# Kernel optimization log

Hardware: AMD Instinct MI355X
Metric: run time of the kernel (lower is better)

## Reference

```python
import jax, jax.numpy as jnp
import numpy as np

NUM_USERS = 100000
NUM_ITEMS = 50000
N_NODES = NUM_USERS + NUM_ITEMS
EMBED_DIM = 64
NUM_LAYERS = 3
NUM_EDGES = 1250000
EDGE_ATTR_DIM = 7
MLP_HID = 32
AUDIO_SCALE = 1.0
META_SCALE = 0.5


def _l2norm(x, eps=1e-12):
    # F.normalize(p=2, dim=-1): x / max(||x||, eps)
    n = jnp.sqrt(jnp.sum(x * x, axis=-1, keepdims=True))
    return x / jnp.maximum(n, eps)


def setup_inputs() -> dict:
    key = jax.random.key(0)
    ks = jax.random.split(key, 12)
    return {
        'user_emb_w': jax.random.normal(ks[0], (NUM_USERS, EMBED_DIM), jnp.float32),
        'artist_emb_w': jax.random.normal(ks[1], (20000, EMBED_DIM), jnp.float32),
        'album_emb_w': jax.random.normal(ks[2], (40000, EMBED_DIM), jnp.float32),
        'item_audio': jax.random.normal(ks[3], (NUM_ITEMS, EMBED_DIM), jnp.float32),
        'edge_attr': jax.random.normal(ks[4], (NUM_EDGES, EDGE_ATTR_DIM), jnp.float32),
        'edge_weight_init': jax.random.uniform(ks[5], (NUM_EDGES,), jnp.float32),
        'w1': jax.random.normal(ks[6], (EDGE_ATTR_DIM + 1, MLP_HID), jnp.float32),
        'b1': jnp.zeros((MLP_HID,), jnp.float32),
        'w2': jax.random.normal(ks[7], (MLP_HID, 1), jnp.float32),
        'b2': jnp.zeros((1,), jnp.float32),
        'edge_index': jax.random.randint(ks[8], (2, NUM_EDGES), 0, N_NODES, jnp.int64 if jax.config.read('jax_enable_x64') else jnp.int32),
        'artist_ids': jax.random.randint(ks[9], (NUM_ITEMS,), 0, 20000, jnp.int32),
        'album_ids': jax.random.randint(ks[10], (NUM_ITEMS,), 0, 40000, jnp.int32),
    }


def reference(user_emb_w, artist_emb_w, album_emb_w, item_audio, edge_attr,
              edge_weight_init, w1, b1, w2, b2, edge_index, artist_ids, album_ids):
    # Edge weight MLP: Linear -> ReLU -> Linear -> Sigmoid, squeezed
    ef = jnp.concatenate([edge_attr, edge_weight_init[:, None]], axis=1)  # [E, 8]
    h = jax.nn.relu(ef @ w1 + b1)
    w = jax.nn.sigmoid(h @ w2 + b2)[:, 0]  # [E]

    # Node features
    user_embed = _l2norm(user_emb_w)                                   # [U, D]
    meta = (artist_emb_w[artist_ids] + album_emb_w[album_ids]) * META_SCALE
    item_embed = _l2norm(item_audio * AUDIO_SCALE + meta)              # [I, D]
    x = jnp.concatenate([user_embed, item_embed], axis=0)              # [N, D]

    # gcn_norm (LGConv default, no self-loops): deg from target (col) scatter of w
    row, col = edge_index[0], edge_index[1]
    deg = jax.ops.segment_sum(w, col, num_segments=N_NODES)
    dinv = jnp.where(deg > 0, jax.lax.rsqrt(jnp.maximum(deg, 1e-30)), 0.0)
    norm = dinv[row] * w * dinv[col]                                   # [E]

    acc = x
    for _ in range(NUM_LAYERS):
        msg = norm[:, None] * x[row]                                   # [E, D]
        x = jax.ops.segment_sum(msg, col, num_segments=N_NODES)       # [N, D]
        acc = acc + x
    x = _l2norm(acc / (NUM_LAYERS + 1))

    user_emb = x[:NUM_USERS]
    item_emb = x[NUM_USERS:]
    align_loss = jnp.float32(0.0)
    return user_emb, item_emb, align_loss
```

## Files before the change

kernel.cpp:

```cpp
#include <hip/hip_runtime.h>
#include <hip/hip_bf16.h>
#include <math.h>

#define NUM_USERS  100000
#define NUM_ITEMS  50000
#define N_NODES    150000
#define EMBED_DIM  64
#define NUM_EDGES  1250000
#define MLP_HID    32
#define SCAN_B     1024
#define SCAN_NB    ((N_NODES + SCAN_B - 1) / SCAN_B)
#define NPW        4
#define PAD(x)     (((x) + 7) & ~7)

__global__ void hist_mlp(const float* __restrict__ edge_attr,
                         const float* __restrict__ ew,
                         const float* __restrict__ w1,
                         const float* __restrict__ b1,
                         const float* __restrict__ w2,
                         const float* __restrict__ b2,
                         const int*   __restrict__ edge_index,
                         int*  __restrict__ cnt,
                         int*  __restrict__ rank,
                         int2* __restrict__ epair) {
    __shared__ float w1s[8 * MLP_HID];
    __shared__ float b1s[MLP_HID];
    __shared__ float w2s[MLP_HID];
    int tid = threadIdx.x;
    if (tid < 8 * MLP_HID) w1s[tid] = w1[tid];
    if (tid < MLP_HID) { b1s[tid] = b1[tid]; w2s[tid] = w2[tid]; }
    __syncthreads();

    int e = blockIdx.x * blockDim.x + tid;
    if (e >= NUM_EDGES) return;

    int c = edge_index[NUM_EDGES + e];
    rank[e] = atomicAdd(&cnt[c], 1);

    float ef[8];
#pragma unroll
    for (int k = 0; k < 7; ++k) ef[k] = edge_attr[e * 7 + k];
    ef[7] = ew[e];

    float s = b2[0];
#pragma unroll
    for (int j = 0; j < MLP_HID; ++j) {
        float h = b1s[j];
#pragma unroll
        for (int k = 0; k < 8; ++k) h = fmaf(ef[k], w1s[k * MLP_HID + j], h);
        h = fmaxf(h, 0.0f);
        s = fmaf(h, w2s[j], s);
    }
    float w = 1.0f / (1.0f + expf(-s));

    int2 pr;
    pr.x = edge_index[e];
    pr.y = __float_as_int(w);
    epair[e] = pr;
}

__global__ void scan_partial(const int* __restrict__ cnt,
                             int* __restrict__ part) {
    __shared__ int s[SCAN_B];
    int tid = threadIdx.x;
    int i = blockIdx.x * SCAN_B + tid;
    s[tid] = (i < N_NODES) ? PAD(cnt[i]) : 0;
    __syncthreads();
#pragma unroll
    for (int off = SCAN_B / 2; off > 0; off >>= 1) {
        if (tid < off) s[tid] += s[tid + off];
        __syncthreads();
    }
    if (tid == 0) part[blockIdx.x] = s[0];
}

__global__ void scan_offsets(const int* __restrict__ part,
                             int* __restrict__ base_off) {
    __shared__ int s[256];
    int tid = threadIdx.x;
    int v = (tid < SCAN_NB) ? part[tid] : 0;
    s[tid] = v;
    __syncthreads();
#pragma unroll
    for (int off = 1; off < 256; off <<= 1) {
        int t = (tid >= off) ? s[tid - off] : 0;
        __syncthreads();
        s[tid] += t;
        __syncthreads();
    }
    if (tid < SCAN_NB) base_off[tid] = s[tid] - v;
}

__global__ void scan_apply(const int* __restrict__ cnt,
                           const int* __restrict__ base_off,
                           int* __restrict__ row_ptr) {
    __shared__ int s[SCAN_B];
    int tid = threadIdx.x;
    int i = blockIdx.x * SCAN_B + tid;
    int v = (i < N_NODES) ? PAD(cnt[i]) : 0;
    s[tid] = v;
    __syncthreads();
    for (int off = 1; off < SCAN_B; off <<= 1) {
        int t = (tid >= off) ? s[tid - off] : 0;
        __syncthreads();
        s[tid] += t;
        __syncthreads();
    }
    if (i < N_NODES) row_ptr[i] = s[tid] - v + base_off[blockIdx.x];
    if (i == N_NODES - 1) row_ptr[N_NODES] = s[tid] + base_off[blockIdx.x];
}

__global__ void scatter_perm(const int* __restrict__ edge_index,
                             const int* __restrict__ rank,
                             const int* __restrict__ row_ptr,
                             int* __restrict__ perm) {
    int e = blockIdx.x * blockDim.x + threadIdx.x;
    if (e >= NUM_EDGES) return;
    int c = edge_index[NUM_EDGES + e];
    perm[row_ptr[c] + rank[e]] = e;
}

__global__ void pair_build(const int* __restrict__ row_ptr,
                           const int* __restrict__ cnt,
                           const int* __restrict__ perm,
                           const int2* __restrict__ epair,
                           int2* __restrict__ csr_pair,
                           float* __restrict__ dinv) {
    int t = blockIdx.x * blockDim.x + threadIdx.x;
    int node = t >> 4;
    int lane = t & 15;
    if (node >= N_NODES) return;
    int s = row_ptr[node];
    int e = row_ptr[node + 1];
    int re = s + cnt[node];
    float sum = 0.0f;
    for (int j = s + lane; j < e; j += 16) {
        int2 pr;
        if (j < re) {
            int eid = perm[j];
            pr = epair[eid];
            sum += __int_as_float(pr.y);
        } else {
            pr.x = 0; pr.y = 0;
        }
        csr_pair[j] = pr;
    }
    sum += __shfl_xor(sum, 8);
    sum += __shfl_xor(sum, 4);
    sum += __shfl_xor(sum, 2);
    sum += __shfl_xor(sum, 1);
    if (lane == 0)
        dinv[node] = (sum > 0.0f) ? rsqrtf(fmaxf(sum, 1e-30f)) : 0.0f;
}

__global__ void init_x(const float* __restrict__ user_w,
                       const float* __restrict__ artist_w,
                       const float* __restrict__ album_w,
                       const float* __restrict__ audio,
                       const int*   __restrict__ artist_ids,
                       const int*   __restrict__ album_ids,
                       __hip_bfloat16* __restrict__ x) {
    int t = blockIdx.x * blockDim.x + threadIdx.x;
    int row = t >> 6;
    int lane = t & 63;
    if (row >= N_NODES) return;

    float v;
    if (row < NUM_USERS) {
        v = user_w[row * EMBED_DIM + lane];
    } else {
        int r = row - NUM_USERS;
        int ar = artist_ids[r];
        int al = album_ids[r];
        v = audio[r * EMBED_DIM + lane]
          + 0.5f * (artist_w[ar * EMBED_DIM + lane] + album_w[al * EMBED_DIM + lane]);
    }
    float ss = v * v;
#pragma unroll
    for (int off = 32; off > 0; off >>= 1) ss += __shfl_xor(ss, off);
    float scale = 1.0f / fmaxf(sqrtf(ss), 1e-12f);
    x[row * EMBED_DIM + lane] = __float2bfloat16(v * scale);
}

#define BF_LO(u) __uint_as_float((u) << 16)
#define BF_HI(u) __uint_as_float((u) & 0xffff0000u)

__global__ void propagate_mid(const int* __restrict__ row_ptr,
                              const int2* __restrict__ csr_pair,
                              const float* __restrict__ dinv,
                              const unsigned short* __restrict__ xin,
                              unsigned short* __restrict__ xout) {
    int wave = (blockIdx.x * blockDim.x + threadIdx.x) >> 6;
    int lane = threadIdx.x & 63;
    int node0 = wave * NPW;
    if (node0 >= N_NODES) return;

    int eg = lane >> 4;
    int dq = (lane & 15) << 2;

    int rpv = row_ptr[node0 + (lane <= NPW ? lane : NPW)];
    int rs0 = __shfl(rpv, 0);
    int rs1 = __shfl(rpv, 1);
    int rs2 = __shfl(rpv, 2);
    int rs3 = __shfl(rpv, 3);
    int rs4 = __shfl(rpv, 4);

    int j = rs0 + eg;
    int2 pa = csr_pair[j];
    int2 pb = csr_pair[j + 4];

#pragma unroll
    for (int k = 0; k < NPW; ++k) {
        int bs = (k == 0) ? rs0 : (k == 1) ? rs1 : (k == 2) ? rs2 : rs3;
        int be = (k == 0) ? rs1 : (k == 1) ? rs2 : (k == 2) ? rs3 : rs4;
        float a0 = 0, a1 = 0, a2 = 0, a3 = 0;

        for (int base = bs; base < be; base += 8) {
            int   sa = pa.x; float wa = __int_as_float(pa.y);
            int   sb = pb.x; float wb = __int_as_float(pb.y);
            float da = dinv[sa];
            float db = dinv[sb];
            uint2 ua = *(const uint2*)(xin + ((size_t)sa << 6) + dq);
            uint2 ub = *(const uint2*)(xin + ((size_t)sb << 6) + dq);

            j += 8;
            pa = csr_pair[j];
            pb = csr_pair[j + 4];

            float fa = wa * da;
            float fb = wb * db;
            a0 = fmaf(fa, BF_LO(ua.x), a0); a1 = fmaf(fa, BF_HI(ua.x), a1);
            a2 = fmaf(fa, BF_LO(ua.y), a2); a3 = fmaf(fa, BF_HI(ua.y), a3);
            a0 = fmaf(fb, BF_LO(ub.x), a0); a1 = fmaf(fb, BF_HI(ub.x), a1);
            a2 = fmaf(fb, BF_LO(ub.y), a2); a3 = fmaf(fb, BF_HI(ub.y), a3);
        }

        a0 += __shfl_xor(a0, 16); a1 += __shfl_xor(a1, 16);
        a2 += __shfl_xor(a2, 16); a3 += __shfl_xor(a3, 16);
        a0 += __shfl_xor(a0, 32); a1 += __shfl_xor(a1, 32);
        a2 += __shfl_xor(a2, 32); a3 += __shfl_xor(a3, 32);

        if (eg == 0) {
            float dc = dinv[node0 + k];
            size_t o = ((size_t)(node0 + k) << 6) + dq;
            unsigned int b0 = (unsigned int)__bfloat16_as_ushort(__float2bfloat16(a0 * dc));
            unsigned int b1 = (unsigned int)__bfloat16_as_ushort(__float2bfloat16(a1 * dc));
            unsigned int b2 = (unsigned int)__bfloat16_as_ushort(__float2bfloat16(a2 * dc));
            unsigned int b3 = (unsigned int)__bfloat16_as_ushort(__float2bfloat16(a3 * dc));
            uint2 u;
            u.x = b0 | (b1 << 16);
            u.y = b2 | (b3 << 16);
            *(uint2*)(xout + o) = u;
        }
    }
}

__global__ void propagate_final(const int* __restrict__ row_ptr,
                                const int2* __restrict__ csr_pair,
                                const float* __restrict__ dinv,
                                const unsigned short* __restrict__ x0,
                                const unsigned short* __restrict__ x1,
                                const unsigned short* __restrict__ x2,
                                float* __restrict__ outp) {
    int wave = (blockIdx.x * blockDim.x + threadIdx.x) >> 6;
    int lane = threadIdx.x & 63;
    int node0 = wave * NPW;
    if (node0 >= N_NODES) return;

    int eg = lane >> 4;
    int dq = (lane & 15) << 2;

    int rpv = row_ptr[node0 + (lane <= NPW ? lane : NPW)];
    int rs0 = __shfl(rpv, 0);
    int rs1 = __shfl(rpv, 1);
    int rs2 = __shfl(rpv, 2);
    int rs3 = __shfl(rpv, 3);
    int rs4 = __shfl(rpv, 4);

    int j = rs0 + eg;
    int2 pa = csr_pair[j];
    int2 pb = csr_pair[j + 4];

#pragma unroll
    for (int k = 0; k < NPW; ++k) {
        int bs = (k == 0) ? rs0 : (k == 1) ? rs1 : (k == 2) ? rs2 : rs3;
        int be = (k == 0) ? rs1 : (k == 1) ? rs2 : (k == 2) ? rs3 : rs4;
        float a0 = 0, a1 = 0, a2 = 0, a3 = 0;

        for (int base = bs; base < be; base += 8) {
            int   sa = pa.x; float wa = __int_as_float(pa.y);
            int   sb = pb.x; float wb = __int_as_float(pb.y);
            float da = dinv[sa];
            float db = dinv[sb];
            uint2 ua = *(const uint2*)(x2 + ((size_t)sa << 6) + dq);
            uint2 ub = *(const uint2*)(x2 + ((size_t)sb << 6) + dq);

            j += 8;
            pa = csr_pair[j];
            pb = csr_pair[j + 4];

            float fa = wa * da;
            float fb = wb * db;
            a0 = fmaf(fa, BF_LO(ua.x), a0); a1 = fmaf(fa, BF_HI(ua.x), a1);
            a2 = fmaf(fa, BF_LO(ua.y), a2); a3 = fmaf(fa, BF_HI(ua.y), a3);
            a0 = fmaf(fb, BF_LO(ub.x), a0); a1 = fmaf(fb, BF_HI(ub.x), a1);
            a2 = fmaf(fb, BF_LO(ub.y), a2); a3 = fmaf(fb, BF_HI(ub.y), a3);
        }

        a0 += __shfl_xor(a0, 16); a1 += __shfl_xor(a1, 16);
        a2 += __shfl_xor(a2, 16); a3 += __shfl_xor(a3, 16);
        a0 += __shfl_xor(a0, 32); a1 += __shfl_xor(a1, 32);
        a2 += __shfl_xor(a2, 32); a3 += __shfl_xor(a3, 32);

        if (eg == 0) {
            float dc = dinv[node0 + k];
            size_t o = ((size_t)(node0 + k) << 6) + dq;
            uint2 u0 = *(const uint2*)(x0 + o);
            uint2 u1 = *(const uint2*)(x1 + o);
            uint2 u2 = *(const uint2*)(x2 + o);

            float v0 = (BF_LO(u0.x) + BF_LO(u1.x) + BF_LO(u2.x) + a0 * dc) * 0.25f;
            float v1 = (BF_HI(u0.x) + BF_HI(u1.x) + BF_HI(u2.x) + a1 * dc) * 0.25f;
            float v2 = (BF_LO(u0.y) + BF_LO(u1.y) + BF_LO(u2.y) + a2 * dc) * 0.25f;
            float v3 = (BF_HI(u0.y) + BF_HI(u1.y) + BF_HI(u2.y) + a3 * dc) * 0.25f;

            float ss = v0 * v0 + v1 * v1 + v2 * v2 + v3 * v3;
            ss += __shfl_xor(ss, 1);
            ss += __shfl_xor(ss, 2);
            ss += __shfl_xor(ss, 4);
            ss += __shfl_xor(ss, 8);
            float scale = 1.0f / fmaxf(sqrtf(ss), 1e-12f);

            float4 r = { v0 * scale, v1 * scale, v2 * scale, v3 * scale };
            *(float4*)(outp + o) = r;
        }
    }
    if (blockIdx.x == 0 && threadIdx.x == 0)
        outp[(size_t)N_NODES * EMBED_DIM] = 0.0f;
}

#undef BF_LO
#undef BF_HI

extern "C" void kernel_launch(void* const* d_in, const int* in_sizes, int n_in,
                              void* d_out, int out_size, void* d_ws, size_t ws_size,
                              hipStream_t stream) {
    const float* user_w     = (const float*)d_in[0];
    const float* artist_w   = (const float*)d_in[1];
    const float* album_w    = (const float*)d_in[2];
    const float* audio      = (const float*)d_in[3];
    const float* edge_attr  = (const float*)d_in[4];
    const float* ew         = (const float*)d_in[5];
    const float* w1         = (const float*)d_in[6];
    const float* b1         = (const float*)d_in[7];
    const float* w2         = (const float*)d_in[8];
    const float* b2         = (const float*)d_in[9];
    const int*   edge_index = (const int*)d_in[10];
    const int*   artist_ids = (const int*)d_in[11];
    const int*   album_ids  = (const int*)d_in[12];
    float* out = (float*)d_out;

    float* ws = (float*)d_ws;
    unsigned short* x0 = (unsigned short*)ws;
    unsigned short* x1 = (unsigned short*)(ws + 4800000);
    unsigned short* x2 = (unsigned short*)(ws + 9600000);
    float* dinv    = ws + 14400000;
    int*  row_ptr  = (int*)(ws + 14560000);
    int2* csr_pair = (int2*)(ws + 14720000);
    int*   cnt     = (int*)ws;
    int*   rank    = (int*)(ws + 150000);
    int*   part    = (int*)(ws + 1400000);
    int*   baseoff = (int*)(ws + 1401000);
    int2*  epair   = (int2*)(ws + 1500000);
    int*   perm    = (int*)(ws + 4800000);

    const int B = 256;
    const int egrid   = (NUM_EDGES + B - 1) / B;
    const int ngrid   = (N_NODES * EMBED_DIM) / B;
    const int ngrid16 = (N_NODES * 16) / B;
    const int pgrid   = (N_NODES / NPW * 64) / B;

    hipMemsetAsync(cnt, 0, N_NODES * sizeof(int), stream);

    hist_mlp<<<egrid, B, 0, stream>>>(
        edge_attr, ew, w1, b1, w2, b2, edge_index, cnt, rank, epair);

    scan_partial<<<SCAN_NB, SCAN_B, 0, stream>>>(cnt, part);
    scan_offsets<<<1, 256, 0, stream>>>(part, baseoff);
    scan_apply<<<SCAN_NB, SCAN_B, 0, stream>>>(cnt, baseoff, row_ptr);

    scatter_perm<<<egrid, B, 0, stream>>>(edge_index, rank, row_ptr, perm);

    pair_build<<<ngrid16, B, 0, stream>>>(
        row_ptr, cnt, perm, epair, csr_pair, dinv);

    init_x<<<ngrid, B, 0, stream>>>(
        user_w, artist_w, album_w, audio, artist_ids, album_ids,
        (__hip_bfloat16*)x0);

    propagate_mid<<<pgrid, B, 0, stream>>>(row_ptr, csr_pair, dinv, x0, x1);
    propagate_mid<<<pgrid, B, 0, stream>>>(row_ptr, csr_pair, dinv, x1, x2);
    propagate_final<<<pgrid, B, 0, stream>>>(row_ptr, csr_pair, dinv, x0, x1, x2, out);
}
```

Measured before the change: 401.2 us.

## Precompute full edge norm in CSR and stream edges across nodes in propagation

Degree is now accumulated with float atomics in the MLP kernel, and a separate kernel computes dinv before CSR build. The symmetric norm dinv[row]*w*dinv[col] is folded into each CSR pair, so the propagation kernels no longer gather dinv per edge or scale per node. The propagation loop is restructured to walk a wave's four nodes' edges as one contiguous stream with 16-edge padding, 4 edges per lane group and a deeper software prefetch. It also pads CSR rows to 16 entries, which adds dummy edges, and uses atomic float adds whose summation order is nondeterministic.

```diff
diff --git a/kernel.cpp b/kernel.cpp
--- a/kernel.cpp
+++ b/kernel.cpp
@@ -11,7 +11,7 @@
 #define SCAN_B     1024
 #define SCAN_NB    ((N_NODES + SCAN_B - 1) / SCAN_B)
 #define NPW        4
-#define PAD(x)     (((x) + 7) & ~7)
+#define PAD(x)     (((x) + 15) & ~15)
 
 __global__ void hist_mlp(const float* __restrict__ edge_attr,
                          const float* __restrict__ ew,
@@ -20,9 +20,10 @@
                          const float* __restrict__ w2,
                          const float* __restrict__ b2,
                          const int*   __restrict__ edge_index,
-                         int*  __restrict__ cnt,
-                         int*  __restrict__ rank,
-                         int2* __restrict__ epair) {
+                         int*   __restrict__ cnt,
+                         float* __restrict__ deg,
+                         int*   __restrict__ rank,
+                         int2*  __restrict__ epair) {
     __shared__ float w1s[8 * MLP_HID];
     __shared__ float b1s[MLP_HID];
     __shared__ float w2s[MLP_HID];
@@ -52,6 +53,8 @@
         s = fmaf(h, w2s[j], s);
     }
     float w = 1.0f / (1.0f + expf(-s));
+
+    atomicAdd(&deg[c], w);
 
     int2 pr;
     pr.x = edge_index[e];
@@ -110,6 +113,22 @@
     if (i == N_NODES - 1) row_ptr[N_NODES] = s[tid] + base_off[blockIdx.x];
 }
 
+__global__ void make_dinv(const float* __restrict__ deg,
+                          float* __restrict__ dinv,
+                          const int* __restrict__ row_ptr,
+                          int2* __restrict__ csr_pair) {
+    int t = blockIdx.x * blockDim.x + threadIdx.x;
+    if (t < N_NODES) {
+        float d = deg[t];
+        dinv[t] = (d > 0.0f) ? rsqrtf(fmaxf(d, 1e-30f)) : 0.0f;
+    }
+    if (t < 64) {
+        int end = row_ptr[N_NODES];
+        int2 z; z.x = 0; z.y = 0;
+        csr_pair[end + t] = z;
+    }
+}
+
 __global__ void scatter_perm(const int* __restrict__ edge_index,
                              const int* __restrict__ rank,
                              const int* __restrict__ row_ptr,
@@ -124,8 +143,8 @@
                            const int* __restrict__ cnt,
                            const int* __restrict__ perm,
                            const int2* __restrict__ epair,
-                           int2* __restrict__ csr_pair,
-                           float* __restrict__ dinv) {
+                           const float* __restrict__ dinv,
+                           int2* __restrict__ csr_pair) {
     int t = blockIdx.x * blockDim.x + threadIdx.x;
     int node = t >> 4;
     int lane = t & 15;
@@ -133,24 +152,18 @@
     int s = row_ptr[node];
     int e = row_ptr[node + 1];
     int re = s + cnt[node];
-    float sum = 0.0f;
+    float dc = dinv[node];
     for (int j = s + lane; j < e; j += 16) {
         int2 pr;
         if (j < re) {
             int eid = perm[j];
             pr = epair[eid];
-            sum += __int_as_float(pr.y);
+            pr.y = __float_as_int(__int_as_float(pr.y) * dc * dinv[pr.x]);
         } else {
             pr.x = 0; pr.y = 0;
         }
         csr_pair[j] = pr;
     }
-    sum += __shfl_xor(sum, 8);
-    sum += __shfl_xor(sum, 4);
-    sum += __shfl_xor(sum, 2);
-    sum += __shfl_xor(sum, 1);
-    if (lane == 0)
-        dinv[node] = (sum > 0.0f) ? rsqrtf(fmaxf(sum, 1e-30f)) : 0.0f;
 }
 
 __global__ void init_x(const float* __restrict__ user_w,
@@ -185,9 +198,16 @@
 #define BF_LO(u) __uint_as_float((u) << 16)
 #define BF_HI(u) __uint_as_float((u) & 0xffff0000u)
 
+#define REDUCE_ACC()                                                         \
+    a0 += __shfl_xor(a0, 16); a1 += __shfl_xor(a1, 16);                      \
+    a2 += __shfl_xor(a2, 16); a3 += __shfl_xor(a3, 16);                      \
+    a0 += __shfl_xor(a0, 32); a1 += __shfl_xor(a1, 32);                      \
+    a2 += __shfl_xor(a2, 32); a3 += __shfl_xor(a3, 32)
+
+#define NEXT_BOUND() ((k == 1) ? rs2 : (k == 2) ? rs3 : rs4)
+
 __global__ void propagate_mid(const int* __restrict__ row_ptr,
                               const int2* __restrict__ csr_pair,
-                              const float* __restrict__ dinv,
                               const unsigned short* __restrict__ xin,
                               unsigned short* __restrict__ xout) {
     int wave = (blockIdx.x * blockDim.x + threadIdx.x) >> 6;
@@ -205,59 +225,86 @@
     int rs3 = __shfl(rpv, 3);
     int rs4 = __shfl(rpv, 4);
 
-    int j = rs0 + eg;
-    int2 pa = csr_pair[j];
-    int2 pb = csr_pair[j + 4];
-
-#pragma unroll
-    for (int k = 0; k < NPW; ++k) {
-        int bs = (k == 0) ? rs0 : (k == 1) ? rs1 : (k == 2) ? rs2 : rs3;
-        int be = (k == 0) ? rs1 : (k == 1) ? rs2 : (k == 2) ? rs3 : rs4;
-        float a0 = 0, a1 = 0, a2 = 0, a3 = 0;
-
-        for (int base = bs; base < be; base += 8) {
-            int   sa = pa.x; float wa = __int_as_float(pa.y);
-            int   sb = pb.x; float wb = __int_as_float(pb.y);
-            float da = dinv[sa];
-            float db = dinv[sb];
-            uint2 ua = *(const uint2*)(xin + ((size_t)sa << 6) + dq);
-            uint2 ub = *(const uint2*)(xin + ((size_t)sb << 6) + dq);
-
-            j += 8;
-            pa = csr_pair[j];
-            pb = csr_pair[j + 4];
-
-            float fa = wa * da;
-            float fb = wb * db;
-            a0 = fmaf(fa, BF_LO(ua.x), a0); a1 = fmaf(fa, BF_HI(ua.x), a1);
-            a2 = fmaf(fa, BF_LO(ua.y), a2); a3 = fmaf(fa, BF_HI(ua.y), a3);
-            a0 = fmaf(fb, BF_LO(ub.x), a0); a1 = fmaf(fb, BF_HI(ub.x), a1);
-            a2 = fmaf(fb, BF_LO(ub.y), a2); a3 = fmaf(fb, BF_HI(ub.y), a3);
+    float a0 = 0, a1 = 0, a2 = 0, a3 = 0;
+    int k = 0;
+    int bnext = rs1;
+
+#define STORE_MID()                                                          \
+    do {                                                                     \
+        if (eg == 0) {                                                       \
+            size_t o = ((size_t)(node0 + k) << 6) + dq;                      \
+            unsigned int b0 = (unsigned int)__bfloat16_as_ushort(__float2bfloat16(a0)); \
+            unsigned int b1 = (unsigned int)__bfloat16_as_ushort(__float2bfloat16(a1)); \
+            unsigned int b2 = (unsigned int)__bfloat16_as_ushort(__float2bfloat16(a2)); \
+            unsigned int b3 = (unsigned int)__bfloat16_as_ushort(__float2bfloat16(a3)); \
+            uint2 u;                                                         \
+            u.x = b0 | (b1 << 16);                                           \
+            u.y = b2 | (b3 << 16);                                           \
+            *(uint2*)(xout + o) = u;                                         \
+        }                                                                    \
+    } while (0)
+
+    while (k < NPW && rs0 == bnext) {
+        STORE_MID();
+        ++k;
+        bnext = NEXT_BOUND();
+    }
+
+    int j = rs0 + (eg << 2);
+    int2 pa0 = csr_pair[j],      pa1 = csr_pair[j + 1];
+    int2 pa2 = csr_pair[j + 2],  pa3 = csr_pair[j + 3];
+    uint2 ua0 = *(const uint2*)(xin + ((size_t)pa0.x << 6) + dq);
+    uint2 ua1 = *(const uint2*)(xin + ((size_t)pa1.x << 6) + dq);
+    uint2 ua2 = *(const uint2*)(xin + ((size_t)pa2.x << 6) + dq);
+    uint2 ua3 = *(const uint2*)(xin + ((size_t)pa3.x << 6) + dq);
+    int2 pb0 = csr_pair[j + 16], pb1 = csr_pair[j + 17];
+    int2 pb2 = csr_pair[j + 18], pb3 = csr_pair[j + 19];
+
+    for (int base = rs0; base < rs4; base += 16) {
+        bool live = (base + 16) < rs4;
+        int sb0 = live ? pb0.x : 0;
+        int sb1 = live ? pb1.x : 0;
+        int sb2 = live ? pb2.x : 0;
+        int sb3 = live ? pb3.x : 0;
+        uint2 ub0 = *(const uint2*)(xin + ((size_t)sb0 << 6) + dq);
+        uint2 ub1 = *(const uint2*)(xin + ((size_t)sb1 << 6) + dq);
+        uint2 ub2 = *(const uint2*)(xin + ((size_t)sb2 << 6) + dq);
+        uint2 ub3 = *(const uint2*)(xin + ((size_t)sb3 << 6) + dq);
+        int2 pc0 = csr_pair[j + 32], pc1 = csr_pair[j + 33];
+        int2 pc2 = csr_pair[j + 34], pc3 = csr_pair[j + 35];
+
+        float w0 = __int_as_float(pa0.y);
+        float w1 = __int_as_float(pa1.y);
+        float w2 = __int_as_float(pa2.y);
+        float w3 = __int_as_float(pa3.y);
+        a0 = fmaf(w0, BF_LO(ua0.x), a0); a1 = fmaf(w0, BF_HI(ua0.x), a1);
+        a2 = fmaf(w0, BF_LO(ua0.y), a2); a3 = fmaf(w0, BF_HI(ua0.y), a3);
+        a0 = fmaf(w1, BF_LO(ua1.x), a0); a1 = fmaf(w1, BF_HI(ua1.x), a1);
+        a2 = fmaf(w1, BF_LO(ua1.y), a2); a3 = fmaf(w1, BF_HI(ua1.y), a3);
+        a0 = fmaf(w2, BF_LO(ua2.x), a0); a1 = fmaf(w2, BF_HI(ua2.x), a1);
+        a2 = fmaf(w2, BF_LO(ua2.y), a2); a3 = fmaf(w2, BF_HI(ua2.y), a3);
+        a0 = fmaf(w3, BF_LO(ua3.x), a0); a1 = fmaf(w3, BF_HI(ua3.x), a1);
+        a2 = fmaf(w3, BF_LO(ua3.y), a2); a3 = fmaf(w3, BF_HI(ua3.y), a3);
+
+        pa0 = pb0; pa1 = pb1; pa2 = pb2; pa3 = pb3;
+        pb0 = pc0; pb1 = pc1; pb2 = pc2; pb3 = pc3;
+        ua0 = ub0; ua1 = ub1; ua2 = ub2; ua3 = ub3;
+        j += 16;
+
+        int pos = base + 16;
+        while (k < NPW && pos == bnext) {
+            REDUCE_ACC();
+            STORE_MID();
+            a0 = 0; a1 = 0; a2 = 0; a3 = 0;
+            ++k;
+            bnext = NEXT_BOUND();
         }
-
-        a0 += __shfl_xor(a0, 16); a1 += __shfl_xor(a1, 16);
-        a2 += __shfl_xor(a2, 16); a3 += __shfl_xor(a3, 16);
-        a0 += __shfl_xor(a0, 32); a1 += __shfl_xor(a1, 32);
-        a2 += __shfl_xor(a2, 32); a3 += __shfl_xor(a3, 32);
-
-        if (eg == 0) {
-            float dc = dinv[node0 + k];
-            size_t o = ((size_t)(node0 + k) << 6) + dq;
-            unsigned int b0 = (unsigned int)__bfloat16_as_ushort(__float2bfloat16(a0 * dc));
-            unsigned int b1 = (unsigned int)__bfloat16_as_ushort(__float2bfloat16(a1 * dc));
-            unsigned int b2 = (unsigned int)__bfloat16_as_ushort(__float2bfloat16(a2 * dc));
-            unsigned int b3 = (unsigned int)__bfloat16_as_ushort(__float2bfloat16(a3 * dc));
-            uint2 u;
-            u.x = b0 | (b1 << 16);
-            u.y = b2 | (b3 << 16);
-            *(uint2*)(xout + o) = u;
-        }
-    }
+    }
+#undef STORE_MID
 }
 
 __global__ void propagate_final(const int* __restrict__ row_ptr,
                                 const int2* __restrict__ csr_pair,
-                                const float* __restrict__ dinv,
                                 const unsigned short* __restrict__ x0,
                                 const unsigned short* __restrict__ x1,
                                 const unsigned short* __restrict__ x2,
@@ -277,64 +324,89 @@
     int rs3 = __shfl(rpv, 3);
     int rs4 = __shfl(rpv, 4);
 
-    int j = rs0 + eg;
-    int2 pa = csr_pair[j];
-    int2 pb = csr_pair[j + 4];
-
-#pragma unroll
-    for (int k = 0; k < NPW; ++k) {
-        int bs = (k == 0) ? rs0 : (k == 1) ? rs1 : (k == 2) ? rs2 : rs3;
-        int be = (k == 0) ? rs1 : (k == 1) ? rs2 : (k == 2) ? rs3 : rs4;
-        float a0 = 0, a1 = 0, a2 = 0, a3 = 0;
-
-        for (int base = bs; base < be; base += 8) {
-            int   sa = pa.x; float wa = __int_as_float(pa.y);
-            int   sb = pb.x; float wb = __int_as_float(pb.y);
-            float da = dinv[sa];
-            float db = dinv[sb];
-            uint2 ua = *(const uint2*)(x2 + ((size_t)sa << 6) + dq);
-            uint2 ub = *(const uint2*)(x2 + ((size_t)sb << 6) + dq);
-
-            j += 8;
-            pa = csr_pair[j];
-            pb = csr_pair[j + 4];
-
-            float fa = wa * da;
-            float fb = wb * db;
-            a0 = fmaf(fa, BF_LO(ua.x), a0); a1 = fmaf(fa, BF_HI(ua.x), a1);
-            a2 = fmaf(fa, BF_LO(ua.y), a2); a3 = fmaf(fa, BF_HI(ua.y), a3);
-            a0 = fmaf(fb, BF_LO(ub.x), a0); a1 = fmaf(fb, BF_HI(ub.x), a1);
-            a2 = fmaf(fb, BF_LO(ub.y), a2); a3 = fmaf(fb, BF_HI(ub.y), a3);
+    float a0 = 0, a1 = 0, a2 = 0, a3 = 0;
+    int k = 0;
+    int bnext = rs1;
+
+#define STORE_FIN()                                                          \
+    do {                                                                     \
+        if (eg == 0) {                                                       \
+            size_t o = ((size_t)(node0 + k) << 6) + dq;                      \
+            uint2 u0 = *(const uint2*)(x0 + o);                              \
+            uint2 u1 = *(const uint2*)(x1 + o);                              \
+            uint2 u2 = *(const uint2*)(x2 + o);                              \
+            float v0 = (BF_LO(u0.x) + BF_LO(u1.x) + BF_LO(u2.x) + a0) * 0.25f; \
+            float v1 = (BF_HI(u0.x) + BF_HI(u1.x) + BF_HI(u2.x) + a1) * 0.25f; \
+            float v2 = (BF_LO(u0.y) + BF_LO(u1.y) + BF_LO(u2.y) + a2) * 0.25f; \
+            float v3 = (BF_HI(u0.y) + BF_HI(u1.y) + BF_HI(u2.y) + a3) * 0.25f; \
+            float ss = v0 * v0 + v1 * v1 + v2 * v2 + v3 * v3;                \
+            ss += __shfl_xor(ss, 1);                                         \
+            ss += __shfl_xor(ss, 2);                                         \
+            ss += __shfl_xor(ss, 4);                                         \
+            ss += __shfl_xor(ss, 8);                                         \
+            float scale = 1.0f / fmaxf(sqrtf(ss), 1e-12f);                   \
+            float4 r = { v0 * scale, v1 * scale, v2 * scale, v3 * scale };   \
+            *(float4*)(outp + o) = r;                                        \
+        }                                                                    \
+    } while (0)
+
+    while (k < NPW && rs0 == bnext) {
+        STORE_FIN();
+        ++k;
+        bnext = NEXT_BOUND();
+    }
+
+    int j = rs0 + (eg << 2);
+    int2 pa0 = csr_pair[j],      pa1 = csr_pair[j + 1];
+    int2 pa2 = csr_pair[j + 2],  pa3 = csr_pair[j + 3];
+    uint2 ua0 = *(const uint2*)(x2 + ((size_t)pa0.x << 6) + dq);
+    uint2 ua1 = *(const uint2*)(x2 + ((size_t)pa1.x << 6) + dq);
+    uint2 ua2 = *(const uint2*)(x2 + ((size_t)pa2.x << 6) + dq);
+    uint2 ua3 = *(const uint2*)(x2 + ((size_t)pa3.x << 6) + dq);
+    int2 pb0 = csr_pair[j + 16], pb1 = csr_pair[j + 17];
+    int2 pb2 = csr_pair[j + 18], pb3 = csr_pair[j + 19];
+
+    for (int base = rs0; base < rs4; base += 16) {
+        bool live = (base + 16) < rs4;
+        int sb0 = live ? pb0.x : 0;
+        int sb1 = live ? pb1.x : 0;
+        int sb2 = live ? pb2.x : 0;
+        int sb3 = live ? pb3.x : 0;
+        uint2 ub0 = *(const uint2*)(x2 + ((size_t)sb0 << 6) + dq);
+        uint2 ub1 = *(const uint2*)(x2 + ((size_t)sb1 << 6) + dq);
+        uint2 ub2 = *(const uint2*)(x2 + ((size_t)sb2 << 6) + dq);
+        uint2 ub3 = *(const uint2*)(x2 + ((size_t)sb3 << 6) + dq);
+        int2 pc0 = csr_pair[j + 32], pc1 = csr_pair[j + 33];
+        int2 pc2 = csr_pair[j + 34], pc3 = csr_pair[j + 35];
+
+        float w0 = __int_as_float(pa0.y);
+        float w1 = __int_as_float(pa1.y);
+        float w2 = __int_as_float(pa2.y);
+        float w3 = __int_as_float(pa3.y);
+        a0 = fmaf(w0, BF_LO(ua0.x), a0); a1 = fmaf(w0, BF_HI(ua0.x), a1);
+        a2 = fmaf(w0, BF_LO(ua0.y), a2); a3 = fmaf(w0, BF_HI(ua0.y), a3);
+        a0 = fmaf(w1, BF_LO(ua1.x), a0); a1 = fmaf(w1, BF_HI(ua1.x), a1);
+        a2 = fmaf(w1, BF_LO(ua1.y), a2); a3 = fmaf(w1, BF_HI(ua1.y), a3);
+        a0 = fmaf(w2, BF_LO(ua2.x), a0); a1 = fmaf(w2, BF_HI(ua2.x), a1);
+        a2 = fmaf(w2, BF_LO(ua2.y), a2); a3 = fmaf(w2, BF_HI(ua2.y), a3);
+        a0 = fmaf(w3, BF_LO(ua3.x), a0); a1 = fmaf(w3, BF_HI(ua3.x), a1);
+        a2 = fmaf(w3, BF_LO(ua3.y), a2); a3 = fmaf(w3, BF_HI(ua3.y), a3);
+
+        pa0 = pb0; pa1 = pb1; pa2 = pb2; pa3 = pb3;
+        pb0 = pc0; pb1 = pc1; pb2 = pc2; pb3 = pc3;
+        ua0 = ub0; ua1 = ub1; ua2 = ub2; ua3 = ub3;
+        j += 16;
+
+        int pos = base + 16;
+        while (k < NPW && pos == bnext) {
+            REDUCE_ACC();
+            STORE_FIN();
+            a0 = 0; a1 = 0; a2 = 0; a3 = 0;
+            ++k;
+            bnext = NEXT_BOUND();
         }
-
-        a0 += __shfl_xor(a0, 16); a1 += __shfl_xor(a1, 16);
-        a2 += __shfl_xor(a2, 16); a3 += __shfl_xor(a3, 16);
-        a0 += __shfl_xor(a0, 32); a1 += __shfl_xor(a1, 32);
-        a2 += __shfl_xor(a2, 32); a3 += __shfl_xor(a3, 32);
-
-        if (eg == 0) {
-            float dc = dinv[node0 + k];
-            size_t o = ((size_t)(node0 + k) << 6) + dq;
-            uint2 u0 = *(const uint2*)(x0 + o);
-            uint2 u1 = *(const uint2*)(x1 + o);
-            uint2 u2 = *(const uint2*)(x2 + o);
-
-            float v0 = (BF_LO(u0.x) + BF_LO(u1.x) + BF_LO(u2.x) + a0 * dc) * 0.25f;
-            float v1 = (BF_HI(u0.x) + BF_HI(u1.x) + BF_HI(u2.x) + a1 * dc) * 0.25f;
-            float v2 = (BF_LO(u0.y) + BF_LO(u1.y) + BF_LO(u2.y) + a2 * dc) * 0.25f;
-            float v3 = (BF_HI(u0.y) + BF_HI(u1.y) + BF_HI(u2.y) + a3 * dc) * 0.25f;
-
-            float ss = v0 * v0 + v1 * v1 + v2 * v2 + v3 * v3;
-            ss += __shfl_xor(ss, 1);
-            ss += __shfl_xor(ss, 2);
-            ss += __shfl_xor(ss, 4);
-            ss += __shfl_xor(ss, 8);
-            float scale = 1.0f / fmaxf(sqrtf(ss), 1e-12f);
-
-            float4 r = { v0 * scale, v1 * scale, v2 * scale, v3 * scale };
-            *(float4*)(outp + o) = r;
-        }
-    }
+    }
+#undef STORE_FIN
     if (blockIdx.x == 0 && threadIdx.x == 0)
         outp[(size_t)N_NODES * EMBED_DIM] = 0.0f;
 }
@@ -368,37 +440,41 @@
     int*  row_ptr  = (int*)(ws + 14560000);
     int2* csr_pair = (int2*)(ws + 14720000);
     int*   cnt     = (int*)ws;
-    int*   rank    = (int*)(ws + 150000);
-    int*   part    = (int*)(ws + 1400000);
-    int*   baseoff = (int*)(ws + 1401000);
-    int2*  epair   = (int2*)(ws + 1500000);
+    float* deg     = ws + 150000;
+    int*   rank    = (int*)(ws + 300000);
+    int*   part    = (int*)(ws + 1600000);
+    int*   baseoff = (int*)(ws + 1601000);
+    int2*  epair   = (int2*)(ws + 1700000);
     int*   perm    = (int*)(ws + 4800000);
 
     const int B = 256;
     const int egrid   = (NUM_EDGES + B - 1) / B;
     const int ngrid   = (N_NODES * EMBED_DIM) / B;
     const int ngrid16 = (N_NODES * 16) / B;
+    const int dgrid   = (N_NODES + B - 1) / B;
     const int pgrid   = (N_NODES / NPW * 64) / B;
 
-    hipMemsetAsync(cnt, 0, N_NODES * sizeof(int), stream);
+    hipMemsetAsync(cnt, 0, 2 * N_NODES * sizeof(int), stream);
 
     hist_mlp<<<egrid, B, 0, stream>>>(
-        edge_attr, ew, w1, b1, w2, b2, edge_index, cnt, rank, epair);
+        edge_attr, ew, w1, b1, w2, b2, edge_index, cnt, deg, rank, epair);
 
     scan_partial<<<SCAN_NB, SCAN_B, 0, stream>>>(cnt, part);
     scan_offsets<<<1, 256, 0, stream>>>(part, baseoff);
     scan_apply<<<SCAN_NB, SCAN_B, 0, stream>>>(cnt, baseoff, row_ptr);
 
+    make_dinv<<<dgrid, B, 0, stream>>>(deg, dinv, row_ptr, csr_pair);
+
     scatter_perm<<<egrid, B, 0, stream>>>(edge_index, rank, row_ptr, perm);
 
     pair_build<<<ngrid16, B, 0, stream>>>(
-        row_ptr, cnt, perm, epair, csr_pair, dinv);
+        row_ptr, cnt, perm, epair, dinv, csr_pair);
 
     init_x<<<ngrid, B, 0, stream>>>(
         user_w, artist_w, album_w, audio, artist_ids, album_ids,
         (__hip_bfloat16*)x0);
 
-    propagate_mid<<<pgrid, B, 0, stream>>>(row_ptr, csr_pair, dinv, x0, x1);
-    propagate_mid<<<pgrid, B, 0, stream>>>(row_ptr, csr_pair, dinv, x1, x2);
-    propagate_final<<<pgrid, B, 0, stream>>>(row_ptr, csr_pair, dinv, x0, x1, x2, out);
-}
+    propagate_mid<<<pgrid, B, 0, stream>>>(row_ptr, csr_pair, x0, x1);
+    propagate_mid<<<pgrid, B, 0, stream>>>(row_ptr, csr_pair, x1, x2);
+    propagate_final<<<pgrid, B, 0, stream>>>(row_ptr, csr_pair, x0, x1, x2, out);
+}
```

New measurement: 467.6 us. 16.6% more time.

## Pre-scale propagated features by dinv to drop per-edge source degree gathers

Applied to the files above, without the earlier changes.

Propagation now carries y = dinv * x, so the edge loop no longer gathers dinv[src] per edge and the output is scaled by dinv^2. The final layer recovers x through a stored reciprocal degree, and the initial layer is kept in fp32 in the output buffer. The edge loop now handles 4 contiguous edges per lane with 16-edge padding, and scatter_perm does 4 edges per thread. This removes one random gather per edge, at the cost of more padding work and possible precision drift for small degrees.

```diff
diff --git a/kernel.cpp b/kernel.cpp
--- a/kernel.cpp
+++ b/kernel.cpp
@@ -11,7 +11,7 @@
 #define SCAN_B     1024
 #define SCAN_NB    ((N_NODES + SCAN_B - 1) / SCAN_B)
 #define NPW        4
-#define PAD(x)     (((x) + 7) & ~7)
+#define PAD(x)     (((x) + 15) & ~15)
 
 __global__ void hist_mlp(const float* __restrict__ edge_attr,
                          const float* __restrict__ ew,
@@ -20,9 +20,9 @@
                          const float* __restrict__ w2,
                          const float* __restrict__ b2,
                          const int*   __restrict__ edge_index,
-                         int*  __restrict__ cnt,
-                         int*  __restrict__ rank,
-                         int2* __restrict__ epair) {
+                         int*   __restrict__ cnt,
+                         int*   __restrict__ rank,
+                         int2*  __restrict__ epair) {
     __shared__ float w1s[8 * MLP_HID];
     __shared__ float b1s[MLP_HID];
     __shared__ float w2s[MLP_HID];
@@ -114,10 +114,14 @@
                              const int* __restrict__ rank,
                              const int* __restrict__ row_ptr,
                              int* __restrict__ perm) {
-    int e = blockIdx.x * blockDim.x + threadIdx.x;
+    int t = blockIdx.x * blockDim.x + threadIdx.x;
+    int e = 4 * t;
     if (e >= NUM_EDGES) return;
-    int c = edge_index[NUM_EDGES + e];
-    perm[row_ptr[c] + rank[e]] = e;
+#pragma unroll
+    for (int q = 0; q < 4; ++q) {
+        int c = edge_index[NUM_EDGES + e + q];
+        perm[row_ptr[c] + rank[e + q]] = e + q;
+    }
 }
 
 __global__ void pair_build(const int* __restrict__ row_ptr,
@@ -125,7 +129,9 @@
                            const int* __restrict__ perm,
                            const int2* __restrict__ epair,
                            int2* __restrict__ csr_pair,
-                           float* __restrict__ dinv) {
+                           float* __restrict__ dinv,
+                           float* __restrict__ dinv2,
+                           float* __restrict__ rd) {
     int t = blockIdx.x * blockDim.x + threadIdx.x;
     int node = t >> 4;
     int lane = t & 15;
@@ -149,8 +155,16 @@
     sum += __shfl_xor(sum, 4);
     sum += __shfl_xor(sum, 2);
     sum += __shfl_xor(sum, 1);
-    if (lane == 0)
-        dinv[node] = (sum > 0.0f) ? rsqrtf(fmaxf(sum, 1e-30f)) : 0.0f;
+    if (lane == 0) {
+        float dv = (sum > 0.0f) ? rsqrtf(fmaxf(sum, 1e-30f)) : 0.0f;
+        dinv[node]  = dv;
+        dinv2[node] = dv * dv;
+        rd[node]    = (dv > 0.0f) ? (1.0f / dv) : 0.0f;
+    }
+    if (node == N_NODES - 1) {
+        int2 z; z.x = 0; z.y = 0;
+        for (int q = lane; q < 64; q += 16) csr_pair[e + q] = z;
+    }
 }
 
 __global__ void init_x(const float* __restrict__ user_w,
@@ -159,7 +173,9 @@
                        const float* __restrict__ audio,
                        const int*   __restrict__ artist_ids,
                        const int*   __restrict__ album_ids,
-                       __hip_bfloat16* __restrict__ x) {
+                       const float* __restrict__ dinv,
+                       float* __restrict__ x0out,
+                       unsigned short* __restrict__ y0) {
     int t = blockIdx.x * blockDim.x + threadIdx.x;
     int row = t >> 6;
     int lane = t & 63;
@@ -179,7 +195,10 @@
 #pragma unroll
     for (int off = 32; off > 0; off >>= 1) ss += __shfl_xor(ss, off);
     float scale = 1.0f / fmaxf(sqrtf(ss), 1e-12f);
-    x[row * EMBED_DIM + lane] = __float2bfloat16(v * scale);
+    float x0 = v * scale;
+    size_t o = (size_t)row * EMBED_DIM + lane;
+    x0out[o] = x0;
+    y0[o] = __bfloat16_as_ushort(__float2bfloat16(x0 * dinv[row]));
 }
 
 #define BF_LO(u) __uint_as_float((u) << 16)
@@ -187,9 +206,9 @@
 
 __global__ void propagate_mid(const int* __restrict__ row_ptr,
                               const int2* __restrict__ csr_pair,
-                              const float* __restrict__ dinv,
-                              const unsigned short* __restrict__ xin,
-                              unsigned short* __restrict__ xout) {
+                              const float* __restrict__ dinv2,
+                              const unsigned short* __restrict__ yin,
+                              unsigned short* __restrict__ yout) {
     int wave = (blockIdx.x * blockDim.x + threadIdx.x) >> 6;
     int lane = threadIdx.x & 63;
     int node0 = wave * NPW;
@@ -205,9 +224,11 @@
     int rs3 = __shfl(rpv, 3);
     int rs4 = __shfl(rpv, 4);
 
-    int j = rs0 + eg;
-    int2 pa = csr_pair[j];
-    int2 pb = csr_pair[j + 4];
+    int j = rs0 + (eg << 2);
+    int2 pa0 = csr_pair[j];
+    int2 pa1 = csr_pair[j + 1];
+    int2 pa2 = csr_pair[j + 2];
+    int2 pa3 = csr_pair[j + 3];
 
 #pragma unroll
     for (int k = 0; k < NPW; ++k) {
@@ -215,24 +236,31 @@
         int be = (k == 0) ? rs1 : (k == 1) ? rs2 : (k == 2) ? rs3 : rs4;
         float a0 = 0, a1 = 0, a2 = 0, a3 = 0;
 
-        for (int base = bs; base < be; base += 8) {
-            int   sa = pa.x; float wa = __int_as_float(pa.y);
-            int   sb = pb.x; float wb = __int_as_float(pb.y);
-            float da = dinv[sa];
-            float db = dinv[sb];
-            uint2 ua = *(const uint2*)(xin + ((size_t)sa << 6) + dq);
-            uint2 ub = *(const uint2*)(xin + ((size_t)sb << 6) + dq);
-
-            j += 8;
-            pa = csr_pair[j];
-            pb = csr_pair[j + 4];
-
-            float fa = wa * da;
-            float fb = wb * db;
-            a0 = fmaf(fa, BF_LO(ua.x), a0); a1 = fmaf(fa, BF_HI(ua.x), a1);
-            a2 = fmaf(fa, BF_LO(ua.y), a2); a3 = fmaf(fa, BF_HI(ua.y), a3);
-            a0 = fmaf(fb, BF_LO(ub.x), a0); a1 = fmaf(fb, BF_HI(ub.x), a1);
-            a2 = fmaf(fb, BF_LO(ub.y), a2); a3 = fmaf(fb, BF_HI(ub.y), a3);
+        for (int base = bs; base < be; base += 16) {
+            int   s0 = pa0.x; float w0 = __int_as_float(pa0.y);
+            int   s1 = pa1.x; float w1 = __int_as_float(pa1.y);
+            int   s2 = pa2.x; float w2 = __int_as_float(pa2.y);
+            int   s3 = pa3.x; float w3 = __int_as_float(pa3.y);
+
+            uint2 u0 = *(const uint2*)(yin + ((size_t)s0 << 6) + dq);
+            uint2 u1 = *(const uint2*)(yin + ((size_t)s1 << 6) + dq);
+            uint2 u2 = *(const uint2*)(yin + ((size_t)s2 << 6) + dq);
+            uint2 u3 = *(const uint2*)(yin + ((size_t)s3 << 6) + dq);
+
+            j += 16;
+            pa0 = csr_pair[j];
+            pa1 = csr_pair[j + 1];
+            pa2 = csr_pair[j + 2];
+            pa3 = csr_pair[j + 3];
+
+            a0 = fmaf(w0, BF_LO(u0.x), a0); a1 = fmaf(w0, BF_HI(u0.x), a1);
+            a2 = fmaf(w0, BF_LO(u0.y), a2); a3 = fmaf(w0, BF_HI(u0.y), a3);
+            a0 = fmaf(w1, BF_LO(u1.x), a0); a1 = fmaf(w1, BF_HI(u1.x), a1);
+            a2 = fmaf(w1, BF_LO(u1.y), a2); a3 = fmaf(w1, BF_HI(u1.y), a3);
+            a0 = fmaf(w2, BF_LO(u2.x), a0); a1 = fmaf(w2, BF_HI(u2.x), a1);
+            a2 = fmaf(w2, BF_LO(u2.y), a2); a3 = fmaf(w2, BF_HI(u2.y), a3);
+            a0 = fmaf(w3, BF_LO(u3.x), a0); a1 = fmaf(w3, BF_HI(u3.x), a1);
+            a2 = fmaf(w3, BF_LO(u3.y), a2); a3 = fmaf(w3, BF_HI(u3.y), a3);
         }
 
         a0 += __shfl_xor(a0, 16); a1 += __shfl_xor(a1, 16);
@@ -241,16 +269,16 @@
         a2 += __shfl_xor(a2, 32); a3 += __shfl_xor(a3, 32);
 
         if (eg == 0) {
-            float dc = dinv[node0 + k];
+            float dc2 = dinv2[node0 + k];
             size_t o = ((size_t)(node0 + k) << 6) + dq;
-            unsigned int b0 = (unsigned int)__bfloat16_as_ushort(__float2bfloat16(a0 * dc));
-            unsigned int b1 = (unsigned int)__bfloat16_as_ushort(__float2bfloat16(a1 * dc));
-            unsigned int b2 = (unsigned int)__bfloat16_as_ushort(__float2bfloat16(a2 * dc));
-            unsigned int b3 = (unsigned int)__bfloat16_as_ushort(__float2bfloat16(a3 * dc));
+            unsigned int b0 = (unsigned int)__bfloat16_as_ushort(__float2bfloat16(a0 * dc2));
+            unsigned int b1 = (unsigned int)__bfloat16_as_ushort(__float2bfloat16(a1 * dc2));
+            unsigned int b2 = (unsigned int)__bfloat16_as_ushort(__float2bfloat16(a2 * dc2));
+            unsigned int b3 = (unsigned int)__bfloat16_as_ushort(__float2bfloat16(a3 * dc2));
             uint2 u;
             u.x = b0 | (b1 << 16);
             u.y = b2 | (b3 << 16);
-            *(uint2*)(xout + o) = u;
+            *(uint2*)(yout + o) = u;
         }
     }
 }
@@ -258,9 +286,9 @@
 __global__ void propagate_final(const int* __restrict__ row_ptr,
                                 const int2* __restrict__ csr_pair,
                                 const float* __restrict__ dinv,
-                                const unsigned short* __restrict__ x0,
-                                const unsigned short* __restrict__ x1,
-                                const unsigned short* __restrict__ x2,
+                                const float* __restrict__ rd,
+                                const unsigned short* __restrict__ y1,
+                                const unsigned short* __restrict__ y2,
                                 float* __restrict__ outp) {
     int wave = (blockIdx.x * blockDim.x + threadIdx.x) >> 6;
     int lane = threadIdx.x & 63;
@@ -277,9 +305,11 @@
     int rs3 = __shfl(rpv, 3);
     int rs4 = __shfl(rpv, 4);
 
-    int j = rs0 + eg;
-    int2 pa = csr_pair[j];
-    int2 pb = csr_pair[j + 4];
+    int j = rs0 + (eg << 2);
+    int2 pa0 = csr_pair[j];
+    int2 pa1 = csr_pair[j + 1];
+    int2 pa2 = csr_pair[j + 2];
+    int2 pa3 = csr_pair[j + 3];
 
 #pragma unroll
     for (int k = 0; k < NPW; ++k) {
@@ -287,24 +317,31 @@
         int be = (k == 0) ? rs1 : (k == 1) ? rs2 : (k == 2) ? rs3 : rs4;
         float a0 = 0, a1 = 0, a2 = 0, a3 = 0;
 
-        for (int base = bs; base < be; base += 8) {
-            int   sa = pa.x; float wa = __int_as_float(pa.y);
-            int   sb = pb.x; float wb = __int_as_float(pb.y);
-            float da = dinv[sa];
-            float db = dinv[sb];
-            uint2 ua = *(const uint2*)(x2 + ((size_t)sa << 6) + dq);
-            uint2 ub = *(const uint2*)(x2 + ((size_t)sb << 6) + dq);
-
-            j += 8;
-            pa = csr_pair[j];
-            pb = csr_pair[j + 4];
-
-            float fa = wa * da;
-            float fb = wb * db;
-            a0 = fmaf(fa, BF_LO(ua.x), a0); a1 = fmaf(fa, BF_HI(ua.x), a1);
-            a2 = fmaf(fa, BF_LO(ua.y), a2); a3 = fmaf(fa, BF_HI(ua.y), a3);
-            a0 = fmaf(fb, BF_LO(ub.x), a0); a1 = fmaf(fb, BF_HI(ub.x), a1);
-            a2 = fmaf(fb, BF_LO(ub.y), a2); a3 = fmaf(fb, BF_HI(ub.y), a3);
+        for (int base = bs; base < be; base += 16) {
+            int   s0 = pa0.x; float w0 = __int_as_float(pa0.y);
+            int   s1 = pa1.x; float w1 = __int_as_float(pa1.y);
+            int   s2 = pa2.x; float w2 = __int_as_float(pa2.y);
+            int   s3 = pa3.x; float w3 = __int_as_float(pa3.y);
+
+            uint2 u0 = *(const uint2*)(y2 + ((size_t)s0 << 6) + dq);
+            uint2 u1 = *(const uint2*)(y2 + ((size_t)s1 << 6) + dq);
+            uint2 u2 = *(const uint2*)(y2 + ((size_t)s2 << 6) + dq);
+            uint2 u3 = *(const uint2*)(y2 + ((size_t)s3 << 6) + dq);
+
+            j += 16;
+            pa0 = csr_pair[j];
+            pa1 = csr_pair[j + 1];
+            pa2 = csr_pair[j + 2];
+            pa3 = csr_pair[j + 3];
+
+            a0 = fmaf(w0, BF_LO(u0.x), a0); a1 = fmaf(w0, BF_HI(u0.x), a1);
+            a2 = fmaf(w0, BF_LO(u0.y), a2); a3 = fmaf(w0, BF_HI(u0.y), a3);
+            a0 = fmaf(w1, BF_LO(u1.x), a0); a1 = fmaf(w1, BF_HI(u1.x), a1);
+            a2 = fmaf(w1, BF_LO(u1.y), a2); a3 = fmaf(w1, BF_HI(u1.y), a3);
+            a0 = fmaf(w2, BF_LO(u2.x), a0); a1 = fmaf(w2, BF_HI(u2.x), a1);
+            a2 = fmaf(w2, BF_LO(u2.y), a2); a3 = fmaf(w2, BF_HI(u2.y), a3);
+            a0 = fmaf(w3, BF_LO(u3.x), a0); a1 = fmaf(w3, BF_HI(u3.x), a1);
+            a2 = fmaf(w3, BF_LO(u3.y), a2); a3 = fmaf(w3, BF_HI(u3.y), a3);
         }
 
         a0 += __shfl_xor(a0, 16); a1 += __shfl_xor(a1, 16);
@@ -313,16 +350,18 @@
         a2 += __shfl_xor(a2, 32); a3 += __shfl_xor(a3, 32);
 
         if (eg == 0) {
-            float dc = dinv[node0 + k];
-            size_t o = ((size_t)(node0 + k) << 6) + dq;
-            uint2 u0 = *(const uint2*)(x0 + o);
-            uint2 u1 = *(const uint2*)(x1 + o);
-            uint2 u2 = *(const uint2*)(x2 + o);
-
-            float v0 = (BF_LO(u0.x) + BF_LO(u1.x) + BF_LO(u2.x) + a0 * dc) * 0.25f;
-            float v1 = (BF_HI(u0.x) + BF_HI(u1.x) + BF_HI(u2.x) + a1 * dc) * 0.25f;
-            float v2 = (BF_LO(u0.y) + BF_LO(u1.y) + BF_LO(u2.y) + a2 * dc) * 0.25f;
-            float v3 = (BF_HI(u0.y) + BF_HI(u1.y) + BF_HI(u2.y) + a3 * dc) * 0.25f;
+            int node = node0 + k;
+            float dv  = dinv[node];
+            float rdv = rd[node];
+            size_t o = ((size_t)node << 6) + dq;
+            float4 x0v = *(const float4*)(outp + o);
+            uint2 u1v = *(const uint2*)(y1 + o);
+            uint2 u2v = *(const uint2*)(y2 + o);
+
+            float v0 = (x0v.x + rdv * (BF_LO(u1v.x) + BF_LO(u2v.x)) + dv * a0) * 0.25f;
+            float v1 = (x0v.y + rdv * (BF_HI(u1v.x) + BF_HI(u2v.x)) + dv * a1) * 0.25f;
+            float v2 = (x0v.z + rdv * (BF_LO(u1v.y) + BF_LO(u2v.y)) + dv * a2) * 0.25f;
+            float v3 = (x0v.w + rdv * (BF_HI(u1v.y) + BF_HI(u2v.y)) + dv * a3) * 0.25f;
 
             float ss = v0 * v0 + v1 * v1 + v2 * v2 + v3 * v3;
             ss += __shfl_xor(ss, 1);
@@ -361,21 +400,24 @@
     float* out = (float*)d_out;
 
     float* ws = (float*)d_ws;
-    unsigned short* x0 = (unsigned short*)ws;
-    unsigned short* x1 = (unsigned short*)(ws + 4800000);
-    unsigned short* x2 = (unsigned short*)(ws + 9600000);
+    unsigned short* y0 = (unsigned short*)ws;
+    unsigned short* y1 = (unsigned short*)(ws + 4800000);
+    unsigned short* y2 = (unsigned short*)(ws + 9600000);
     float* dinv    = ws + 14400000;
-    int*  row_ptr  = (int*)(ws + 14560000);
-    int2* csr_pair = (int2*)(ws + 14720000);
+    float* dinv2   = ws + 14560000;
+    float* rd      = ws + 14720000;
+    int*  row_ptr  = (int*)(ws + 14880000);
+    int2* csr_pair = (int2*)(ws + 15040000);
     int*   cnt     = (int*)ws;
     int*   rank    = (int*)(ws + 150000);
-    int*   part    = (int*)(ws + 1400000);
-    int*   baseoff = (int*)(ws + 1401000);
-    int2*  epair   = (int2*)(ws + 1500000);
+    int*   part    = (int*)(ws + 1600000);
+    int*   baseoff = (int*)(ws + 1601000);
+    int2*  epair   = (int2*)(ws + 1700000);
     int*   perm    = (int*)(ws + 4800000);
 
     const int B = 256;
     const int egrid   = (NUM_EDGES + B - 1) / B;
+    const int egrid4  = (NUM_EDGES / 4 + B - 1) / B;
     const int ngrid   = (N_NODES * EMBED_DIM) / B;
     const int ngrid16 = (N_NODES * 16) / B;
     const int pgrid   = (N_NODES / NPW * 64) / B;
@@ -389,16 +431,16 @@
     scan_offsets<<<1, 256, 0, stream>>>(part, baseoff);
     scan_apply<<<SCAN_NB, SCAN_B, 0, stream>>>(cnt, baseoff, row_ptr);
 
-    scatter_perm<<<egrid, B, 0, stream>>>(edge_index, rank, row_ptr, perm);
+    scatter_perm<<<egrid4, B, 0, stream>>>(edge_index, rank, row_ptr, perm);
 
     pair_build<<<ngrid16, B, 0, stream>>>(
-        row_ptr, cnt, perm, epair, csr_pair, dinv);
+        row_ptr, cnt, perm, epair, csr_pair, dinv, dinv2, rd);
 
     init_x<<<ngrid, B, 0, stream>>>(
         user_w, artist_w, album_w, audio, artist_ids, album_ids,
-        (__hip_bfloat16*)x0);
-
-    propagate_mid<<<pgrid, B, 0, stream>>>(row_ptr, csr_pair, dinv, x0, x1);
-    propagate_mid<<<pgrid, B, 0, stream>>>(row_ptr, csr_pair, dinv, x1, x2);
-    propagate_final<<<pgrid, B, 0, stream>>>(row_ptr, csr_pair, dinv, x0, x1, x2, out);
-}
+        dinv, out, y0);
+
+    propagate_mid<<<pgrid, B, 0, stream>>>(row_ptr, csr_pair, dinv2, y0, y1);
+    propagate_mid<<<pgrid, B, 0, stream>>>(row_ptr, csr_pair, dinv2, y1, y2);
+    propagate_final<<<pgrid, B, 0, stream>>>(row_ptr, csr_pair, dinv, rd, y1, y2, out);
+}
```

Result: no change. 401.0 us (-0.0%).
